# Performance work log

Hardware: AMD Instinct MI355X
Metric: run time of the kernel (lower is better)

## Reference

```python
import jax, jax.numpy as jnp
import numpy as np

COL_IDX = 5  # colIdx: column used as sort key
REVERSE = False


def setup_inputs() -> dict:
    key = jax.random.key(0)
    # x: [batch, seq, feat]
    x = jax.random.normal(key, (32, 4096, 256), dtype=jnp.float32)
    return {"x": x}


def reference(x):
    # tf.nn.top_k(x[:, :, nc], k=S) returns indices of a full descending sort
    # with stable tie-breaking (earlier index first). jnp.argsort is stable,
    # so argsort of the negated key reproduces it exactly.
    keys = x[:, :, COL_IDX]                       # [B, S]
    idxs = jnp.argsort(-keys, axis=1)             # [B, S] descending order
    if REVERSE:
        idxs = idxs[:, ::-1]
    # gather_nd with (batch, idx) pairs == take_along_axis over the seq dim
    return jnp.take_along_axis(x, idxs[:, :, None], axis=1)  # [B, S, F]
```

## Files before the change

kernel.cpp:

```cpp
#include <hip/hip_runtime.h>
#include <stdint.h>

#define BATCH   32
#define ROWS    4096
#define COLS    256
#define COL_IDX 5

typedef unsigned long long u64;
typedef unsigned int       u32;

__global__ __launch_bounds__(256)
void extract_keys_kernel(const float* __restrict__ x, u64* __restrict__ keys) {
    const int i = blockIdx.x * 256 + threadIdx.x;
    u32 u = __float_as_uint(x[(size_t)i * COLS + COL_IDX]);
    u = (u >> 31) ? ~u : (u | 0x80000000u);
    u = ~u;
    keys[i] = ((u64)u << 32) | (u32)(i & (ROWS - 1));
}

__global__ __launch_bounds__(256)
void rank_copy_kernel(const float* __restrict__ x,
                      const u64* __restrict__ keys,
                      float* __restrict__ out) {
    const int wave = blockIdx.x * 4 + ((int)threadIdx.x >> 6);
    const int lane = (int)threadIdx.x & 63;
    const int b    = wave >> 6;
    const int r0   = (wave & 63) << 6;
    const u64* kb  = keys + (size_t)b * ROWS;

    const u64 my = kb[r0 + lane];
    int rank = 0;
    for (int j0 = 0; j0 < ROWS; j0 += 64) {
        const u64 kv = kb[j0 + lane];
        const u32 lo = (u32)kv, hi = (u32)(kv >> 32);
        #pragma unroll
        for (int l = 0; l < 64; ++l) {
            const u32 klo = (u32)__builtin_amdgcn_readlane(lo, l);
            const u32 khi = (u32)__builtin_amdgcn_readlane(hi, l);
            const u64 kk  = ((u64)khi << 32) | klo;
            rank += (kk < my) ? 1 : 0;
        }
    }

    const float4* src  = (const float4*)(x   + ((size_t)b * ROWS + r0) * COLS);
    float4*       outb = (float4*)      (out + (size_t)b * ROWS * COLS);
    #pragma unroll 8
    for (int l = 0; l < 64; ++l) {
        const int dst = __builtin_amdgcn_readlane(rank, l);
        outb[(size_t)dst * 64 + lane] = src[l * 64 + lane];
    }
}

extern "C" void kernel_launch(void* const* d_in, const int* in_sizes, int n_in,
                              void* d_out, int out_size, void* d_ws, size_t ws_size,
                              hipStream_t stream) {
    const float* x   = (const float*)d_in[0];
    float*       out = (float*)d_out;
    u64*         keys = (u64*)d_ws;

    extract_keys_kernel<<<(BATCH * ROWS) / 256, 256, 0, stream>>>(x, keys);
    rank_copy_kernel<<<(BATCH * ROWS) / 256, 256, 0, stream>>>(x, keys, out);
}
```

Measured before the change: 302.6 us.

## Split rank counting across four waves per row group with LDS reduction

Each block now handles 64 rows, with its four waves each counting ranks against a quarter of the keys. Partial ranks are summed through shared memory, and each wave scatters 16 of the rows. This quadruples the number of waves in flight to hide latency in the serial compare loop. The cost is a block barrier, a small LDS reduction, and redundant loading of the row keys.

```diff
diff --git a/kernel.cpp b/kernel.cpp
--- a/kernel.cpp
+++ b/kernel.cpp
@@ -18,19 +18,21 @@
     keys[i] = ((u64)u << 32) | (u32)(i & (ROWS - 1));
 }
 
-__global__ __launch_bounds__(256)
+__global__ __launch_bounds__(256, 8)
 void rank_copy_kernel(const float* __restrict__ x,
                       const u64* __restrict__ keys,
                       float* __restrict__ out) {
-    const int wave = blockIdx.x * 4 + ((int)threadIdx.x >> 6);
+    __shared__ int part[4][64];
+    const int w    = (int)threadIdx.x >> 6;
     const int lane = (int)threadIdx.x & 63;
-    const int b    = wave >> 6;
-    const int r0   = (wave & 63) << 6;
-    const u64* kb  = keys + (size_t)b * ROWS;
+    const int b    = blockIdx.x >> 6;
+    const int r0   = (blockIdx.x & 63) << 6;
+    const u64* __restrict__ kb = keys + (size_t)b * ROWS;
 
     const u64 my = kb[r0 + lane];
     int rank = 0;
-    for (int j0 = 0; j0 < ROWS; j0 += 64) {
+    const int jbeg = w * (ROWS / 4);
+    for (int j0 = jbeg; j0 < jbeg + ROWS / 4; j0 += 64) {
         const u64 kv = kb[j0 + lane];
         const u32 lo = (u32)kv, hi = (u32)(kv >> 32);
         #pragma unroll
@@ -41,13 +43,19 @@
             rank += (kk < my) ? 1 : 0;
         }
     }
+    part[w][lane] = rank;
+    __syncthreads();
+    const int total = part[0][lane] + part[1][lane]
+                    + part[2][lane] + part[3][lane];
 
-    const float4* src  = (const float4*)(x   + ((size_t)b * ROWS + r0) * COLS);
-    float4*       outb = (float4*)      (out + (size_t)b * ROWS * COLS);
-    #pragma unroll 8
-    for (int l = 0; l < 64; ++l) {
-        const int dst = __builtin_amdgcn_readlane(rank, l);
-        outb[(size_t)dst * 64 + lane] = src[l * 64 + lane];
+    const float4* __restrict__ src  =
+        (const float4*)(x + ((size_t)b * ROWS + r0) * COLS);
+    float4* __restrict__ outb = (float4*)(out + (size_t)b * ROWS * COLS);
+    #pragma unroll 4
+    for (int t = 0; t < 16; ++t) {
+        const int l   = w * 16 + t;
+        const int dst = __builtin_amdgcn_readlane(total, l);
+        outb[(size_t)dst * 64 + lane] = src[(size_t)l * 64 + lane];
     }
 }
 
@@ -59,5 +67,5 @@
     u64*         keys = (u64*)d_ws;
 
     extract_keys_kernel<<<(BATCH * ROWS) / 256, 256, 0, stream>>>(x, keys);
-    rank_copy_kernel<<<(BATCH * ROWS) / 256, 256, 0, stream>>>(x, keys, out);
+    rank_copy_kernel<<<BATCH * 64, 256, 0, stream>>>(x, keys, out);
 }
```

New measurement: 248.5 us. -17.9%, faster.
